# Kernel optimization log

Measured on AMD Instinct MI355X. Metric: run time of the kernel, lower is better.

## Reference

```python
import jax, jax.numpy as jnp
import numpy as np

B, S, D, FF, E, TOP_K = 4, 2048, 1024, 4096, 8, 2


def setup_inputs() -> dict:
    key = jax.random.key(0)
    ks = jax.random.split(key, 13)
    sd = 1.0 / np.sqrt(D)
    sf = 1.0 / np.sqrt(FF)
    return {
        "x":   jax.random.normal(ks[0], (B, S, D), jnp.float32),
        # parallel 2-way router
        "Wr":  jax.random.normal(ks[1], (D, 2), jnp.float32) * sd,
        "br":  jnp.zeros((2,), jnp.float32),
        # MoE gate
        "Wg":  jax.random.normal(ks[2], (D, E), jnp.float32) * sd,
        "bg":  jnp.zeros((E,), jnp.float32),
        # expert FFNs
        "W1":  jax.random.normal(ks[3], (E, D, FF), jnp.float32) * sd,
        "b1":  jnp.zeros((E, FF), jnp.float32),
        "W2":  jax.random.normal(ks[4], (E, FF, D), jnp.float32) * sf,
        "b2":  jnp.zeros((E, D), jnp.float32),
        # dense FFN
        "D1":  jax.random.normal(ks[5], (D, FF), jnp.float32) * sd,
        "d1b": jnp.zeros((FF,), jnp.float32),
        "D2":  jax.random.normal(ks[6], (FF, D), jnp.float32) * sf,
        "d2b": jnp.zeros((D,), jnp.float32),
    }


def _hybrid_moe(x, Wr, br, Wg, bg, W1, b1, W2, b2, D1, d1b, D2, d2b):
    b, s, d = x.shape
    t = x.reshape(-1, d)                                  # [T, D]
    T = t.shape[0]

    # parallel 2-way blend router
    rp = jax.nn.softmax(x @ Wr + br, axis=-1)             # [B, S, 2]

    # MoE gating: softmax over experts, top-k, renormalize
    gp = jax.nn.softmax(t @ Wg + bg, axis=-1)             # [T, E]
    vals, idx = jax.lax.top_k(gp, TOP_K)                  # [T, K]
    vals = vals / jnp.sum(vals, axis=-1, keepdims=True)
    cw = jnp.zeros((T, E), t.dtype).at[jnp.arange(T)[:, None], idx].add(vals)  # [T, E]

    # expert FFNs (ReLU MLP), combined with top-k weights
    h = jax.nn.relu(jnp.einsum('td,edf->tef', t, W1) + b1)       # [T, E, FF]
    eo = jnp.einsum('tef,efd->ted', h, W2) + b2                  # [T, E, D]
    moe = jnp.einsum('te,ted->td', cw, eo).reshape(b, s, d)

    # dense FFN branch
    dense = jax.nn.relu(x @ D1 + d1b) @ D2 + d2b

    return rp[..., 0:1] * moe + rp[..., 1:2] * dense


def reference(x, Wr, br, Wg, bg, W1, b1, W2, b2, D1, d1b, D2, d2b):
    return _hybrid_moe(x, Wr, br, Wg, bg, W1, b1, W2, b2, D1, d1b, D2, d2b)
```

## Files before the change

### kernel.cpp

```cpp
#include <hip/hip_runtime.h>
#include <stdint.h>

#define T_TOK   8192
#define D_DIM   1024
#define FF_DIM  4096
#define E_NUM   8
#define SLOT_MAX 18432
#define RT_MAX  104

typedef unsigned int   u32;
typedef unsigned short u16;
typedef __attribute__((ext_vector_type(4))) float  f32x4;
typedef __attribute__((ext_vector_type(4))) float  f4;
typedef __attribute__((ext_vector_type(8))) short  bf16x8;
typedef __attribute__((ext_vector_type(8))) unsigned short u16x8;

__device__ __forceinline__ u16 f2bf(float f) {
  u32 u = __builtin_bit_cast(u32, f);
  return (u16)((u + 0x7fffu + ((u >> 16) & 1u)) >> 16);
}
__device__ __forceinline__ float bf2f(u16 h) {
  u32 u = ((u32)h) << 16; return __builtin_bit_cast(float, u);
}

typedef const __attribute__((address_space(1))) u32* gp1_t;
typedef __attribute__((address_space(3))) u32*       lp3_t;
__device__ __forceinline__ void gload16(const u16* g, u16* l) {
  __builtin_amdgcn_global_load_lds((gp1_t)(const void*)g, (lp3_t)l, 16, 0, 0);
}

__global__ void k_init(int* hdr) { if (threadIdx.x < 64) hdr[threadIdx.x] = 0; }

__global__ __launch_bounds__(256) void k_route(
    const float* __restrict__ x, const float* __restrict__ Wr, const float* __restrict__ br,
    const float* __restrict__ Wg, const float* __restrict__ bg,
    int* __restrict__ hdr, int4* __restrict__ tok_sel, float4* __restrict__ tok_wf)
{
  int w = threadIdx.x >> 6, l = threadIdx.x & 63;
  int t = blockIdx.x * 4 + w;
  const float* xt = x + (size_t)t * D_DIM;
  float p[10];
  #pragma unroll
  for (int i = 0; i < 10; ++i) p[i] = 0.f;
  for (int j = 0; j < D_DIM / 64; ++j) {
    int d = j * 64 + l;
    float xv = xt[d];
    p[0] += xv * Wr[d * 2 + 0];
    p[1] += xv * Wr[d * 2 + 1];
    f4 g0 = *(const f4*)&Wg[d * 8];
    f4 g1 = *(const f4*)&Wg[d * 8 + 4];
    p[2] += xv * g0[0]; p[3] += xv * g0[1]; p[4] += xv * g0[2]; p[5] += xv * g0[3];
    p[6] += xv * g1[0]; p[7] += xv * g1[1]; p[8] += xv * g1[2]; p[9] += xv * g1[3];
  }
  #pragma unroll
  for (int off = 32; off; off >>= 1) {
    #pragma unroll
    for (int i = 0; i < 10; ++i) p[i] += __shfl_xor(p[i], off, 64);
  }
  if (l == 0) {
    float a0 = p[0] + br[0], a1 = p[1] + br[1];
    float m  = fmaxf(a0, a1);
    float e0 = __expf(a0 - m), e1 = __expf(a1 - m);
    float rs = 1.f / (e0 + e1);
    float rp0 = e0 * rs, rp1 = e1 * rs;
    float g[E_NUM]; float gm = -1e30f;
    #pragma unroll
    for (int e = 0; e < E_NUM; ++e) { g[e] = p[2 + e] + bg[e]; gm = fmaxf(gm, g[e]); }
    int i0 = 0;
    #pragma unroll
    for (int e = 1; e < E_NUM; ++e) if (g[e] > g[i0]) i0 = e;
    int i1 = (i0 == 0) ? 1 : 0;
    #pragma unroll
    for (int e = 0; e < E_NUM; ++e) if (e != i0 && g[e] > g[i1]) i1 = e;
    float x0 = __expf(g[i0] - gm), x1 = __expf(g[i1] - gm);
    float s = 1.f / (x0 + x1);
    int r0 = atomicAdd(&hdr[i0], 1);
    int r1 = atomicAdd(&hdr[i1], 1);
    tok_sel[t] = make_int4(i0, r0, i1, r1);
    tok_wf[t]  = make_float4(x0 * s, x1 * s, rp0, rp1);
  }
}

__global__ __launch_bounds__(256) void k_offsets(int* __restrict__ hdr,
                                                 int4* __restrict__ tilemap,
                                                 int* __restrict__ perm)
{
  __shared__ int soff[E_NUM + 1];
  int tid = threadIdx.x;
  if (tid == 0) {
    int acc = 0;
    for (int e = 0; e < E_NUM; ++e) {
      soff[e] = acc; hdr[8 + e] = acc;
      acc += (hdr[e] + 255) & ~255;
    }
    soff[E_NUM] = acc;
    hdr[16] = acc;
    hdr[17] = acc >> 8;
    hdr[18] = (acc >> 8) + T_TOK / 256;
  }
  __syncthreads();
  int nmoe = soff[E_NUM] >> 8;
  for (int rt = tid; rt < RT_MAX; rt += 256) {
    int4 ent;
    if (rt < nmoe) {
      int row0 = rt * 256;
      int e = 0;
      while (e < E_NUM - 1 && row0 >= soff[e + 1]) ++e;
      ent = make_int4(0, row0, e, 0);
    } else if (rt < nmoe + T_TOK / 256) {
      ent = make_int4(1, (rt - nmoe) * 256, -1, 0);
    } else {
      ent = make_int4(-1, 0, 0, 0);
    }
    tilemap[rt] = ent;
  }
  for (int s = tid; s < SLOT_MAX; s += 256) perm[s] = -1;
}

__global__ void k_scatter(const int4* __restrict__ tok_sel, const int* __restrict__ hdr,
                          int* __restrict__ perm, int2* __restrict__ tok_slot)
{
  int t = blockIdx.x * 256 + threadIdx.x;
  if (t >= T_TOK) return;
  int4 s = tok_sel[t];
  int s0 = hdr[8 + s.x] + s.y;
  int s1 = hdr[8 + s.z] + s.w;
  perm[s0] = t; perm[s1] = t;
  tok_slot[t] = make_int2(s0, s1);
}

__global__ void k_cast(const float* __restrict__ x, u16* __restrict__ xb, int n8) {
  int i = blockIdx.x * 256 + threadIdx.x;
  if (i >= n8) return;
  const f4* src = (const f4*)x + (size_t)i * 2;
  f4 a = src[0], b = src[1];
  u16x8 o;
  o[0]=f2bf(a[0]); o[1]=f2bf(a[1]); o[2]=f2bf(a[2]); o[3]=f2bf(a[3]);
  o[4]=f2bf(b[0]); o[5]=f2bf(b[1]); o[6]=f2bf(b[2]); o[7]=f2bf(b[3]);
  ((u16x8*)xb)[i] = o;
}

__global__ __launch_bounds__(256) void k_gather(const u16* __restrict__ xb,
                                                const int* __restrict__ perm,
                                                const int* __restrict__ hdr,
                                                u16* __restrict__ xg)
{
  int nslots = hdr[16];
  int row = blockIdx.x * 2 + (threadIdx.x >> 7);
  if (row >= nslots) return;
  int lane = threadIdx.x & 127;
  int t = perm[row];
  u16x8* dst = (u16x8*)(xg + (size_t)row * D_DIM) + lane;
  if (t < 0) { u16x8 z = {0,0,0,0,0,0,0,0}; *dst = z; }
  else       { *dst = *((const u16x8*)(xb + (size_t)t * D_DIM) + lane); }
}

__global__ __launch_bounds__(256) void k_tcast(const float* __restrict__ src,
                                               u16* __restrict__ dst, int R, int C)
{
  const float* s = src + (size_t)blockIdx.z * R * C;
  u16* d = dst + (size_t)blockIdx.z * R * C;
  __shared__ float tile[64][65];
  int tr = blockIdx.y, tc = blockIdx.x;
  int t = threadIdx.x;
  #pragma unroll
  for (int p = 0; p < 4; ++p) {
    int r = p * 16 + (t >> 4);
    int c4 = (t & 15) * 4;
    f4 v = *(const f4*)&s[(size_t)(tr * 64 + r) * C + tc * 64 + c4];
    tile[r][c4+0] = v[0]; tile[r][c4+1] = v[1]; tile[r][c4+2] = v[2]; tile[r][c4+3] = v[3];
  }
  __syncthreads();
  #pragma unroll
  for (int q = 0; q < 2; ++q) {
    int oc = q * 32 + (t >> 3);
    int r8 = (t & 7) * 8;
    u16x8 o;
    #pragma unroll
    for (int j = 0; j < 8; ++j) o[j] = f2bf(tile[r8 + j][oc]);
    *(u16x8*)&d[(size_t)(tc * 64 + oc) * R + tr * 64 + r8] = o;
  }
}

#define LGKM0() { asm volatile("s_waitcnt lgkmcnt(0)" ::: "memory"); \
                  __builtin_amdgcn_sched_barrier(0); }
#define BAR()   __builtin_amdgcn_s_barrier()

template <int RELU>
__global__ __launch_bounds__(512, 2) void k_gemm8p(
    const u16* __restrict__ Amoe, const u16* __restrict__ Aden,
    const u16* __restrict__ Bexp, const u16* __restrict__ Bden,
    const float* __restrict__ biasexp, const float* __restrict__ biasden,
    u16* __restrict__ Omoe, u16* __restrict__ Oden,
    const int* __restrict__ hdr, const int4* __restrict__ tilemap,
    int K, int N, long bexp_stride, int biasexp_stride, int lg2gx)
{
  int gx  = 1 << lg2gx;
  int nwg = gx * gridDim.y;
  int lin = blockIdx.y * gx + blockIdx.x;
  int sw  = (lin & 7) * (nwg >> 3) + (lin >> 3);
  int ct  = sw & (gx - 1);
  int rt  = sw >> lg2gx;
  if (rt >= hdr[18]) return;

  int4 ent = tilemap[rt];
  const u16* A; const u16* B; const float* bias; u16* O;
  if (ent.x == 1) { A = Aden; B = Bden; bias = biasden; O = Oden; }
  else {
    A = Amoe; B = Bexp + (size_t)ent.z * bexp_stride;
    bias = biasexp + (size_t)ent.z * biasexp_stride;
    O = Omoe;
  }
  const int row0 = ent.y;

  __shared__ __align__(16) u16 lds[65536];

  const int tid = threadIdx.x;
  const int wid = tid >> 6, l = tid & 63;
  const int wm = wid >> 2, wn = wid & 3;

  const int skel = ((l & 7) ^ (l >> 3)) * 8;
  const u16* aStage = A + (size_t)(row0     + wid * 8 + (l >> 3)) * K + skel;
  const u16* bStage = B + (size_t)(ct * 256 + wid * 8 + (l >> 3)) * K + skel;

  const int fr = l & 15, fq = l >> 4;
  const int fx = (l & 7) << 4;
  const int cs0 = (fq * 16) ^ fx;
  const int cs1 = (64 + fq * 16) ^ fx;
  const char* ldsc = (const char*)lds;

  auto STAGE_A = [&](int tt, int h, int bb) {
    const u16* src = aStage + (size_t)(h * 128) * K + (size_t)tt * 64;
    u16* dst = &lds[(bb * 2 + h) * 8192 + wid * 512];
    gload16(src, dst);
    gload16(src + (size_t)64 * K, dst + 4096);
  };
  auto STAGE_B = [&](int tt, int h, int bb) {
    const u16* src = bStage + (size_t)(h * 128) * K + (size_t)tt * 64;
    u16* dst = &lds[32768 + (bb * 2 + h) * 8192 + wid * 512];
    gload16(src, dst);
    gload16(src + (size_t)64 * K, dst + 4096);
  };

  f32x4 acc[8][4];
  #pragma unroll
  for (int m = 0; m < 8; ++m)
    #pragma unroll
    for (int n = 0; n < 4; ++n) acc[m][n] = (f32x4){0.f, 0.f, 0.f, 0.f};

  const int NK = K >> 6;

  STAGE_B(0, 0, 0); STAGE_B(0, 1, 0); STAGE_A(0, 0, 0); STAGE_A(0, 1, 0);
  STAGE_B(1, 0, 1); STAGE_B(1, 1, 1); STAGE_A(1, 0, 1);
  asm volatile("s_waitcnt vmcnt(6)" ::: "memory");
  BAR();

  bf16x8 a0[4][2], a1[4][2], b0[2][2], b1[2][2];

  for (int t = 0; t < NK; ++t) {
    const int b = t & 1;
    const char* Areg = ldsc + (size_t)(b * 2 + wm) * 16384;
    const char* Breg = ldsc + 65536 + (size_t)(b * 2 + (wn >> 1)) * 16384;
    const int brow = (wn & 1) * 64;

    #pragma unroll
    for (int j = 0; j < 4; ++j) {
      a0[j][0] = *(const bf16x8*)(Areg + (j * 16 + fr) * 128 + cs0);
      a0[j][1] = *(const bf16x8*)(Areg + (j * 16 + fr) * 128 + cs1);
    }
    #pragma unroll
    for (int i = 0; i < 2; ++i) {
      b0[i][0] = *(const bf16x8*)(Breg + (brow + i * 16 + fr) * 128 + cs0);
      b0[i][1] = *(const bf16x8*)(Breg + (brow + i * 16 + fr) * 128 + cs1);
    }
    if (t + 1 < NK) STAGE_A(t + 1, 1, b ^ 1);
    BAR(); LGKM0();
    __builtin_amdgcn_s_setprio(1);
    #pragma unroll
    for (int j = 0; j < 4; ++j)
      #pragma unroll
      for (int i = 0; i < 2; ++i) {
        acc[j][i] = __builtin_amdgcn_mfma_f32_16x16x32_bf16(a0[j][0], b0[i][0], acc[j][i], 0, 0, 0);
        acc[j][i] = __builtin_amdgcn_mfma_f32_16x16x32_bf16(a0[j][1], b0[i][1], acc[j][i], 0, 0, 0);
      }
    __builtin_amdgcn_s_setprio(0);
    BAR();

    #pragma unroll
    for (int i = 0; i < 2; ++i) {
      b1[i][0] = *(const bf16x8*)(Breg + (brow + 32 + i * 16 + fr) * 128 + cs0);
      b1[i][1] = *(const bf16x8*)(Breg + (brow + 32 + i * 16 + fr) * 128 + cs1);
    }
    BAR(); LGKM0();
    __builtin_amdgcn_s_setprio(1);
    #pragma unroll
    for (int j = 0; j < 4; ++j)
      #pragma unroll
      for (int i = 0; i < 2; ++i) {
        acc[j][2 + i] = __builtin_amdgcn_mfma_f32_16x16x32_bf16(a0[j][0], b1[i][0], acc[j][2 + i], 0, 0, 0);
        acc[j][2 + i] = __builtin_amdgcn_mfma_f32_16x16x32_bf16(a0[j][1], b1[i][1], acc[j][2 + i], 0, 0, 0);
      }
    __builtin_amdgcn_s_setprio(0);
    BAR();

    #pragma unroll
    for (int j = 0; j < 4; ++j) {
      a1[j][0] = *(const bf16x8*)(Areg + (64 + j * 16 + fr) * 128 + cs0);
      a1[j][1] = *(const bf16x8*)(Areg + (64 + j * 16 + fr) * 128 + cs1);
    }
    if (t + 2 < NK) STAGE_B(t + 2, 0, b);
    BAR(); LGKM0();
    __builtin_amdgcn_s_setprio(1);
    #pragma unroll
    for (int j = 0; j < 4; ++j)
      #pragma unroll
      for (int i = 0; i < 2; ++i) {
        acc[4 + j][2 + i] = __builtin_amdgcn_mfma_f32_16x16x32_bf16(a1[j][0], b1[i][0], acc[4 + j][2 + i], 0, 0, 0);
        acc[4 + j][2 + i] = __builtin_amdgcn_mfma_f32_16x16x32_bf16(a1[j][1], b1[i][1], acc[4 + j][2 + i], 0, 0, 0);
      }
    __builtin_amdgcn_s_setprio(0);
    BAR();

    if (t + 2 < NK) { STAGE_B(t + 2, 1, b); STAGE_A(t + 2, 0, b); }
    BAR();
    __builtin_amdgcn_s_setprio(1);
    #pragma unroll
    for (int j = 0; j < 4; ++j)
      #pragma unroll
      for (int i = 0; i < 2; ++i) {
        acc[4 + j][i] = __builtin_amdgcn_mfma_f32_16x16x32_bf16(a1[j][0], b0[i][0], acc[4 + j][i], 0, 0, 0);
        acc[4 + j][i] = __builtin_amdgcn_mfma_f32_16x16x32_bf16(a1[j][1], b0[i][1], acc[4 + j][i], 0, 0, 0);
      }
    __builtin_amdgcn_s_setprio(0);
    if (t < NK - 2) { asm volatile("s_waitcnt vmcnt(6)" ::: "memory"); }
    else            { asm volatile("s_waitcnt vmcnt(0)" ::: "memory"); }
    BAR();
    __builtin_amdgcn_sched_barrier(0);
  }

  __syncthreads();
  float bv[4];
  #pragma unroll
  for (int ni = 0; ni < 4; ++ni) bv[ni] = bias[ct * 256 + wn * 64 + ni * 16 + fr];
  float* ep = (float*)((char*)lds + wid * 4096);
  const int row16 = l >> 2, cg = l & 3;
  #pragma unroll
  for (int mi = 0; mi < 8; ++mi) {
    #pragma unroll
    for (int ni = 0; ni < 4; ++ni) {
      f32x4 v = acc[mi][ni];
      #pragma unroll
      for (int j = 0; j < 4; ++j) {
        float f = v[j] + bv[ni];
        if (RELU) f = fmaxf(f, 0.f);
        ep[(fq * 4 + j) * 64 + ni * 16 + fr] = f;
      }
    }
    #pragma unroll
    for (int p = 0; p < 2; ++p) {
      f4 r0 = *(f4*)&ep[row16 * 64 + (cg + p * 4) * 8];
      f4 r1 = *(f4*)&ep[row16 * 64 + (cg + p * 4) * 8 + 4];
      u16x8 o;
      o[0]=f2bf(r0[0]); o[1]=f2bf(r0[1]); o[2]=f2bf(r0[2]); o[3]=f2bf(r0[3]);
      o[4]=f2bf(r1[0]); o[5]=f2bf(r1[1]); o[6]=f2bf(r1[2]); o[7]=f2bf(r1[3]);
      int rr = row0 + wm * 128 + mi * 16 + row16;
      int cc = ct * 256 + wn * 64 + (cg + p * 4) * 8;
      *(u16x8*)&O[(size_t)rr * N + cc] = o;
    }
  }
}

__global__ __launch_bounds__(128) void k_combine(
    const u16* __restrict__ eo, const u16* __restrict__ dense_o,
    const float4* __restrict__ tok_wf, const int2* __restrict__ tok_slot,
    float* __restrict__ out)
{
  int t = blockIdx.x;
  int c8 = threadIdx.x;
  float4 wf = tok_wf[t];
  int2 sl = tok_slot[t];
  u16x8 a  = *((const u16x8*)(eo + (size_t)sl.x * D_DIM) + c8);
  u16x8 b  = *((const u16x8*)(eo + (size_t)sl.y * D_DIM) + c8);
  u16x8 dn = *((const u16x8*)(dense_o + (size_t)t * D_DIM) + c8);
  float* op = out + (size_t)t * D_DIM + c8 * 8;
  #pragma unroll
  for (int j = 0; j < 8; ++j) {
    float mo = wf.x * bf2f(a[j]) + wf.y * bf2f(b[j]);
    op[j] = wf.z * mo + wf.w * bf2f(dn[j]);
  }
}

extern "C" void kernel_launch(void* const* d_in, const int* in_sizes, int n_in,
                              void* d_out, int out_size, void* d_ws, size_t ws_size,
                              hipStream_t stream)
{
  const float* x   = (const float*)d_in[0];
  const float* Wr  = (const float*)d_in[1];
  const float* br  = (const float*)d_in[2];
  const float* Wg  = (const float*)d_in[3];
  const float* bg  = (const float*)d_in[4];
  const float* W1  = (const float*)d_in[5];
  const float* b1  = (const float*)d_in[6];
  const float* W2  = (const float*)d_in[7];
  const float* b2  = (const float*)d_in[8];
  const float* D1  = (const float*)d_in[9];
  const float* d1b = (const float*)d_in[10];
  const float* D2  = (const float*)d_in[11];
  const float* d2b = (const float*)d_in[12];
  float* out = (float*)d_out;

  char* base = (char*)d_ws;
  size_t cur = 0;
  auto alloc = [&](size_t b) -> void* {
    void* p = base + cur; cur = (cur + b + 255) & ~(size_t)255; return p;
  };
  int*    hdr      = (int*)   alloc(256 * sizeof(int));
  int4*   tilemap  = (int4*)  alloc((size_t)RT_MAX * sizeof(int4));
  int4*   tok_sel  = (int4*)  alloc((size_t)T_TOK * sizeof(int4));
  float4* tok_wf   = (float4*)alloc((size_t)T_TOK * sizeof(float4));
  int2*   tok_slot = (int2*)  alloc((size_t)T_TOK * sizeof(int2));
  int*    perm     = (int*)   alloc((size_t)SLOT_MAX * sizeof(int));
  u16*    xb       = (u16*)   alloc((size_t)T_TOK * D_DIM * 2);
  u16*    xg       = (u16*)   alloc((size_t)SLOT_MAX * D_DIM * 2);
  u16*    W1bt     = (u16*)   alloc((size_t)E_NUM * D_DIM * FF_DIM * 2);
  u16*    W2bt     = (u16*)   alloc((size_t)E_NUM * D_DIM * FF_DIM * 2);
  u16*    D1bt     = (u16*)   alloc((size_t)D_DIM * FF_DIM * 2);
  u16*    D2bt     = (u16*)   alloc((size_t)D_DIM * FF_DIM * 2);
  u16*    h_moe    = (u16*)   alloc((size_t)SLOT_MAX * FF_DIM * 2);
  u16*    h_dense  = (u16*)   alloc((size_t)T_TOK * FF_DIM * 2);
  u16*    eo       = (u16*)   alloc((size_t)SLOT_MAX * D_DIM * 2);
  u16*    dense_o  = (u16*)   alloc((size_t)T_TOK * D_DIM * 2);
  (void)in_sizes; (void)n_in; (void)out_size; (void)ws_size;

  k_init   <<<1, 64, 0, stream>>>(hdr);
  k_route  <<<T_TOK / 4, 256, 0, stream>>>(x, Wr, br, Wg, bg, hdr, tok_sel, tok_wf);
  k_offsets<<<1, 256, 0, stream>>>(hdr, tilemap, perm);
  k_scatter<<<T_TOK / 256, 256, 0, stream>>>(tok_sel, hdr, perm, tok_slot);
  k_cast   <<<(T_TOK * D_DIM / 8) / 256, 256, 0, stream>>>(x, xb, T_TOK * D_DIM / 8);
  k_gather <<<SLOT_MAX / 2, 256, 0, stream>>>(xb, perm, hdr, xg);
  k_tcast  <<<dim3(FF_DIM / 64, D_DIM / 64, E_NUM), 256, 0, stream>>>(W1, W1bt, D_DIM, FF_DIM);
  k_tcast  <<<dim3(D_DIM / 64, FF_DIM / 64, E_NUM), 256, 0, stream>>>(W2, W2bt, FF_DIM, D_DIM);
  k_tcast  <<<dim3(FF_DIM / 64, D_DIM / 64, 1), 256, 0, stream>>>(D1, D1bt, D_DIM, FF_DIM);
  k_tcast  <<<dim3(D_DIM / 64, FF_DIM / 64, 1), 256, 0, stream>>>(D2, D2bt, FF_DIM, D_DIM);

  k_gemm8p<1><<<dim3(FF_DIM / 256, RT_MAX), 512, 0, stream>>>(
      xg, xb, W1bt, D1bt, b1, d1b, h_moe, h_dense, hdr, tilemap,
      D_DIM, FF_DIM, (long)D_DIM * FF_DIM, FF_DIM, 4);
  k_gemm8p<0><<<dim3(D_DIM / 256, RT_MAX), 512, 0, stream>>>(
      h_moe, h_dense, W2bt, D2bt, b2, d2b, eo, dense_o, hdr, tilemap,
      FF_DIM, D_DIM, (long)D_DIM * FF_DIM, D_DIM, 2);

  k_combine<<<T_TOK, 128, 0, stream>>>(eo, dense_o, tok_wf, tok_slot, out);
}
```

Baseline: 796.0 us.

## Software-pipeline LDS fragment reads with MFMA quadrants and pad epilogue staging

Restructures the GEMM main loop so the LDS fragment reads for the next quadrant (and the next k-tile's A0/B0) are issued before or alongside the current quadrant's MFMAs. Each quadrant no longer waits on a barrier plus lgkmcnt before it can compute. This drops one barrier per phase and overlaps LDS latency with matrix math. Separately, the epilogue staging buffer stride is padded from 64 to 68 floats to reduce LDS bank conflicts. In exchange it holds more fragment registers live and makes the synchronisation ordering more delicate.

```diff
diff --git a/kernel.cpp b/kernel.cpp
--- a/kernel.cpp
+++ b/kernel.cpp
@@ -228,6 +228,7 @@
   const int cs0 = (fq * 16) ^ fx;
   const int cs1 = (64 + fq * 16) ^ fx;
   const char* ldsc = (const char*)lds;
+  const int brow = (wn & 1) * 64;
 
   auto STAGE_A = [&](int tt, int h, int bb) {
     const u16* src = aStage + (size_t)(h * 128) * K + (size_t)tt * 64;
@@ -248,101 +249,71 @@
     #pragma unroll
     for (int n = 0; n < 4; ++n) acc[m][n] = (f32x4){0.f, 0.f, 0.f, 0.f};
 
+  bf16x8 a0[4][2], a1[4][2], b0[2][2], b1[2][2];
+
+  #define READ_A0(bb) { const char* Ar = ldsc + (size_t)((bb) * 2 + wm) * 16384; \
+    _Pragma("unroll") for (int j = 0; j < 4; ++j) { \
+      a0[j][0] = *(const bf16x8*)(Ar + (j * 16 + fr) * 128 + cs0); \
+      a0[j][1] = *(const bf16x8*)(Ar + (j * 16 + fr) * 128 + cs1); } }
+  #define READ_A1(bb) { const char* Ar = ldsc + (size_t)((bb) * 2 + wm) * 16384; \
+    _Pragma("unroll") for (int j = 0; j < 4; ++j) { \
+      a1[j][0] = *(const bf16x8*)(Ar + (64 + j * 16 + fr) * 128 + cs0); \
+      a1[j][1] = *(const bf16x8*)(Ar + (64 + j * 16 + fr) * 128 + cs1); } }
+  #define READ_B0(bb) { const char* Br = ldsc + 65536 + (size_t)((bb) * 2 + (wn >> 1)) * 16384; \
+    _Pragma("unroll") for (int i = 0; i < 2; ++i) { \
+      b0[i][0] = *(const bf16x8*)(Br + (brow + i * 16 + fr) * 128 + cs0); \
+      b0[i][1] = *(const bf16x8*)(Br + (brow + i * 16 + fr) * 128 + cs1); } }
+  #define READ_B1(bb) { const char* Br = ldsc + 65536 + (size_t)((bb) * 2 + (wn >> 1)) * 16384; \
+    _Pragma("unroll") for (int i = 0; i < 2; ++i) { \
+      b1[i][0] = *(const bf16x8*)(Br + (brow + 32 + i * 16 + fr) * 128 + cs0); \
+      b1[i][1] = *(const bf16x8*)(Br + (brow + 32 + i * 16 + fr) * 128 + cs1); } }
+  #define MFMA_Q(am, bm, mo, no) { __builtin_amdgcn_s_setprio(1); \
+    _Pragma("unroll") for (int j = 0; j < 4; ++j) \
+      _Pragma("unroll") for (int i = 0; i < 2; ++i) { \
+        acc[(mo) + j][(no) + i] = __builtin_amdgcn_mfma_f32_16x16x32_bf16(am[j][0], bm[i][0], acc[(mo) + j][(no) + i], 0, 0, 0); \
+        acc[(mo) + j][(no) + i] = __builtin_amdgcn_mfma_f32_16x16x32_bf16(am[j][1], bm[i][1], acc[(mo) + j][(no) + i], 0, 0, 0); } \
+    __builtin_amdgcn_s_setprio(0); }
+
   const int NK = K >> 6;
 
   STAGE_B(0, 0, 0); STAGE_B(0, 1, 0); STAGE_A(0, 0, 0); STAGE_A(0, 1, 0);
   STAGE_B(1, 0, 1); STAGE_B(1, 1, 1); STAGE_A(1, 0, 1);
   asm volatile("s_waitcnt vmcnt(6)" ::: "memory");
   BAR();
-
-  bf16x8 a0[4][2], a1[4][2], b0[2][2], b1[2][2];
+  READ_A0(0); READ_B0(0);
 
   for (int t = 0; t < NK; ++t) {
     const int b = t & 1;
-    const char* Areg = ldsc + (size_t)(b * 2 + wm) * 16384;
-    const char* Breg = ldsc + 65536 + (size_t)(b * 2 + (wn >> 1)) * 16384;
-    const int brow = (wn & 1) * 64;
-
-    #pragma unroll
-    for (int j = 0; j < 4; ++j) {
-      a0[j][0] = *(const bf16x8*)(Areg + (j * 16 + fr) * 128 + cs0);
-      a0[j][1] = *(const bf16x8*)(Areg + (j * 16 + fr) * 128 + cs1);
+    READ_B1(b);
+    if (t + 1 < NK) STAGE_A(t + 1, 1, b ^ 1);
+    MFMA_Q(a0, b0, 0, 0);
+    LGKM0();
+    BAR();
+    READ_A1(b);
+    if (t + 2 < NK) STAGE_B(t + 2, 0, b);
+    MFMA_Q(a0, b1, 0, 2);
+    LGKM0();
+    BAR();
+    if (t + 2 < NK) { STAGE_B(t + 2, 1, b); STAGE_A(t + 2, 0, b); }
+    MFMA_Q(a1, b1, 4, 2);
+    BAR();
+    if (t + 1 < NK) {
+      if (t + 2 < NK) { asm volatile("s_waitcnt vmcnt(6)" ::: "memory"); }
+      else            { asm volatile("s_waitcnt vmcnt(0)" ::: "memory"); }
+      READ_A0(b ^ 1);
+      MFMA_Q(a1, b0, 4, 0);
+      READ_B0(b ^ 1);
+    } else {
+      MFMA_Q(a1, b0, 4, 0);
     }
-    #pragma unroll
-    for (int i = 0; i < 2; ++i) {
-      b0[i][0] = *(const bf16x8*)(Breg + (brow + i * 16 + fr) * 128 + cs0);
-      b0[i][1] = *(const bf16x8*)(Breg + (brow + i * 16 + fr) * 128 + cs1);
-    }
-    if (t + 1 < NK) STAGE_A(t + 1, 1, b ^ 1);
-    BAR(); LGKM0();
-    __builtin_amdgcn_s_setprio(1);
-    #pragma unroll
-    for (int j = 0; j < 4; ++j)
-      #pragma unroll
-      for (int i = 0; i < 2; ++i) {
-        acc[j][i] = __builtin_amdgcn_mfma_f32_16x16x32_bf16(a0[j][0], b0[i][0], acc[j][i], 0, 0, 0);
-        acc[j][i] = __builtin_amdgcn_mfma_f32_16x16x32_bf16(a0[j][1], b0[i][1], acc[j][i], 0, 0, 0);
-      }
-    __builtin_amdgcn_s_setprio(0);
     BAR();
-
-    #pragma unroll
-    for (int i = 0; i < 2; ++i) {
-      b1[i][0] = *(const bf16x8*)(Breg + (brow + 32 + i * 16 + fr) * 128 + cs0);
-      b1[i][1] = *(const bf16x8*)(Breg + (brow + 32 + i * 16 + fr) * 128 + cs1);
-    }
-    BAR(); LGKM0();
-    __builtin_amdgcn_s_setprio(1);
-    #pragma unroll
-    for (int j = 0; j < 4; ++j)
-      #pragma unroll
-      for (int i = 0; i < 2; ++i) {
-        acc[j][2 + i] = __builtin_amdgcn_mfma_f32_16x16x32_bf16(a0[j][0], b1[i][0], acc[j][2 + i], 0, 0, 0);
-        acc[j][2 + i] = __builtin_amdgcn_mfma_f32_16x16x32_bf16(a0[j][1], b1[i][1], acc[j][2 + i], 0, 0, 0);
-      }
-    __builtin_amdgcn_s_setprio(0);
-    BAR();
-
-    #pragma unroll
-    for (int j = 0; j < 4; ++j) {
-      a1[j][0] = *(const bf16x8*)(Areg + (64 + j * 16 + fr) * 128 + cs0);
-      a1[j][1] = *(const bf16x8*)(Areg + (64 + j * 16 + fr) * 128 + cs1);
-    }
-    if (t + 2 < NK) STAGE_B(t + 2, 0, b);
-    BAR(); LGKM0();
-    __builtin_amdgcn_s_setprio(1);
-    #pragma unroll
-    for (int j = 0; j < 4; ++j)
-      #pragma unroll
-      for (int i = 0; i < 2; ++i) {
-        acc[4 + j][2 + i] = __builtin_amdgcn_mfma_f32_16x16x32_bf16(a1[j][0], b1[i][0], acc[4 + j][2 + i], 0, 0, 0);
-        acc[4 + j][2 + i] = __builtin_amdgcn_mfma_f32_16x16x32_bf16(a1[j][1], b1[i][1], acc[4 + j][2 + i], 0, 0, 0);
-      }
-    __builtin_amdgcn_s_setprio(0);
-    BAR();
-
-    if (t + 2 < NK) { STAGE_B(t + 2, 1, b); STAGE_A(t + 2, 0, b); }
-    BAR();
-    __builtin_amdgcn_s_setprio(1);
-    #pragma unroll
-    for (int j = 0; j < 4; ++j)
-      #pragma unroll
-      for (int i = 0; i < 2; ++i) {
-        acc[4 + j][i] = __builtin_amdgcn_mfma_f32_16x16x32_bf16(a1[j][0], b0[i][0], acc[4 + j][i], 0, 0, 0);
-        acc[4 + j][i] = __builtin_amdgcn_mfma_f32_16x16x32_bf16(a1[j][1], b0[i][1], acc[4 + j][i], 0, 0, 0);
-      }
-    __builtin_amdgcn_s_setprio(0);
-    if (t < NK - 2) { asm volatile("s_waitcnt vmcnt(6)" ::: "memory"); }
-    else            { asm volatile("s_waitcnt vmcnt(0)" ::: "memory"); }
-    BAR();
-    __builtin_amdgcn_sched_barrier(0);
   }
 
   __syncthreads();
   float bv[4];
   #pragma unroll
   for (int ni = 0; ni < 4; ++ni) bv[ni] = bias[ct * 256 + wn * 64 + ni * 16 + fr];
-  float* ep = (float*)((char*)lds + wid * 4096);
+  float* ep = (float*)((char*)lds + wid * 4608);
   const int row16 = l >> 2, cg = l & 3;
   #pragma unroll
   for (int mi = 0; mi < 8; ++mi) {
@@ -353,13 +324,13 @@
       for (int j = 0; j < 4; ++j) {
         float f = v[j] + bv[ni];
         if (RELU) f = fmaxf(f, 0.f);
-        ep[(fq * 4 + j) * 64 + ni * 16 + fr] = f;
+        ep[(fq * 4 + j) * 68 + ni * 16 + fr] = f;
       }
     }
     #pragma unroll
     for (int p = 0; p < 2; ++p) {
-      f4 r0 = *(f4*)&ep[row16 * 64 + (cg + p * 4) * 8];
-      f4 r1 = *(f4*)&ep[row16 * 64 + (cg + p * 4) * 8 + 4];
+      f4 r0 = *(f4*)&ep[row16 * 68 + (cg + p * 4) * 8];
+      f4 r1 = *(f4*)&ep[row16 * 68 + (cg + p * 4) * 8 + 4];
       u16x8 o;
       o[0]=f2bf(r0[0]); o[1]=f2bf(r0[1]); o[2]=f2bf(r0[2]); o[3]=f2bf(r0[3]);
       o[4]=f2bf(r1[0]); o[5]=f2bf(r1[1]); o[6]=f2bf(r1[2]); o[7]=f2bf(r1[3]);
@@ -368,6 +339,11 @@
       *(u16x8*)&O[(size_t)rr * N + cc] = o;
     }
   }
+  #undef READ_A0
+  #undef READ_A1
+  #undef READ_B0
+  #undef READ_B1
+  #undef MFMA_Q
 }
 
 __global__ __launch_bounds__(128) void k_combine(
```

Result: slower. 1.227 ms (+54.2%).
